# Kernel optimization log

Measured on AMD Instinct MI355X. Metric: run time of the kernel, lower is better.

## Reference

```python
import jax, jax.numpy as jnp
import numpy as np

N = 50000      # nodes
E = 800000     # edges (avg degree 16)
F_IN = 512     # input features
H = 64         # hidden
C = 40         # classes
L = 4          # FAConv layers
EPS = 0.2      # args.epsilon


def setup_inputs() -> dict:
    key = jax.random.key(0)
    ks = jax.random.split(key, 8)
    gain = 1.414
    x = jax.random.normal(ks[0], (N, F_IN), jnp.float32)
    edge_index = jax.random.randint(ks[1], (2, E), 0, N, dtype=jnp.int32)
    W1 = jax.random.normal(ks[2], (H, F_IN), jnp.float32) * (gain * np.sqrt(2.0 / (F_IN + H)))
    b1 = jnp.zeros((H,), jnp.float32)
    W2 = jax.random.normal(ks[3], (C, H), jnp.float32) * (gain * np.sqrt(2.0 / (H + C)))
    b2 = jnp.zeros((C,), jnp.float32)
    att_l = jax.random.normal(ks[4], (L, H), jnp.float32) * np.sqrt(2.0 / (1 + H))
    att_r = jax.random.normal(ks[5], (L, H), jnp.float32) * np.sqrt(2.0 / (1 + H))
    return {"x": x, "edge_index": edge_index, "W1": W1, "b1": b1,
            "W2": W2, "b2": b2, "att_l": att_l, "att_r": att_r}


def reference(x, edge_index, W1, b1, W2, b2, att_l, att_r):
    n = x.shape[0]
    src, dst = edge_index[0], edge_index[1]
    # gcn_norm with self-loops (FAConv normalize=True, add_self_loops=True)
    loop = jnp.arange(n, dtype=src.dtype)
    rows = jnp.concatenate([src, loop])  # source j
    cols = jnp.concatenate([dst, loop])  # target i
    deg = jax.ops.segment_sum(jnp.ones_like(cols, dtype=x.dtype), cols, num_segments=n)
    dinv = jnp.where(deg > 0, jax.lax.rsqrt(jnp.maximum(deg, 1e-12)), 0.0)
    norm = dinv[rows] * dinv[cols]  # [E+N]

    # lin1 + relu (dropout inactive in eval)
    h = jax.nn.relu(x @ W1.T + b1)
    raw = h
    for l in range(L):
        al = h @ att_l[l]  # [N] per-source score
        ar = h @ att_r[l]  # [N] per-target score
        a = jnp.tanh(al[rows] + ar[cols])          # [E+N]
        msg = h[rows] * (a * norm)[:, None]        # [E+N, H]
        h = jax.ops.segment_sum(msg, cols, num_segments=n) + EPS * raw
    logits = h @ W2.T + b2
    return jax.nn.log_softmax(logits, axis=1)
```

## Files before the change

kernel.cpp:

```cpp
#include <hip/hip_runtime.h>

#define F_IN 512
#define HDIM 64
#define NCLS 40
#define NLAYER 4
#define EPS_F 0.2f

typedef __attribute__((ext_vector_type(8))) short short8;
typedef __attribute__((ext_vector_type(4))) float f32x4;
typedef __attribute__((ext_vector_type(8))) unsigned short ushort8;
typedef unsigned long long u64;

__device__ __forceinline__ unsigned short f2bf(float f) {
  unsigned u = __float_as_uint(f);
  u += 0x7FFFu + ((u >> 16) & 1u);
  return (unsigned short)(u >> 16);
}
__device__ __forceinline__ float bf2f(unsigned short s) {
  return __uint_as_float(((unsigned)s) << 16);
}

__global__ __launch_bounds__(256) void k_init(int* indeg, int nN) {
  int i = blockIdx.x * 256 + threadIdx.x;
  if (i < nN) indeg[i] = 0;
}

__global__ __launch_bounds__(256) void k_hist(const int* __restrict__ dst, int* indeg,
                                              int* __restrict__ rank, int nE) {
  int e = blockIdx.x * 256 + threadIdx.x;
  if (e < nE) rank[e] = atomicAdd(&indeg[dst[e]], 1);
}

__global__ __launch_bounds__(256) void k_bsum(const int* __restrict__ indeg, int* bsum, int nN) {
  int i0 = blockIdx.x * 512 + threadIdx.x;
  int v = 0;
  if (i0 < nN) v += indeg[i0];
  if (i0 + 256 < nN) v += indeg[i0 + 256];
#pragma unroll
  for (int off = 32; off > 0; off >>= 1) v += __shfl_xor(v, off, 64);
  __shared__ int s[4];
  if ((threadIdx.x & 63) == 0) s[threadIdx.x >> 6] = v;
  __syncthreads();
  if (threadIdx.x == 0) bsum[blockIdx.x] = s[0] + s[1] + s[2] + s[3];
}

__global__ __launch_bounds__(128) void k_bscan(const int* __restrict__ bsum, int* bpre,
                                               int* rowptr, int nblk, int nN, int nE) {
  __shared__ int sb[128];
  int t = threadIdx.x;
  int v = (t < nblk) ? bsum[t] : 0;
  sb[t] = v;
  __syncthreads();
  int acc = v;
  for (int off = 1; off < 128; off <<= 1) {
    int o = (t >= off) ? sb[t - off] : 0;
    __syncthreads();
    acc += o;
    sb[t] = acc;
    __syncthreads();
  }
  if (t < nblk) bpre[t] = acc - v;
  if (t == 0) rowptr[nN] = nE;
}

__global__ __launch_bounds__(512) void k_rowptr(const int* __restrict__ indeg,
                                                const int* __restrict__ bpre,
                                                const float* __restrict__ al,
                                                const float* __restrict__ ar,
                                                int* rowptr, float* dinv,
                                                float2* P, float2* Q, float* selfc, int nN) {
  __shared__ int sb[512];
  int t = threadIdx.x;
  int i = blockIdx.x * 512 + t;
  int v = (i < nN) ? indeg[i] : 0;
  sb[t] = v;
  __syncthreads();
  int acc = v;
  for (int off = 1; off < 512; off <<= 1) {
    int o = (t >= off) ? sb[t - off] : 0;
    __syncthreads();
    acc += o;
    sb[t] = acc;
    __syncthreads();
  }
  if (i < nN) {
    rowptr[i] = bpre[blockIdx.x] + acc - v;
    float dv = rsqrtf((float)v + 1.0f);
    dinv[i] = dv;
    float a = al[i], r = ar[i];
    P[i] = make_float2(a, dv);
    Q[i] = make_float2(r, dv);
    selfc[i] = tanhf(a + r) * dv * dv;
  }
}

__global__ __launch_bounds__(256) void k_scatter(const int* __restrict__ src,
                                                 const int* __restrict__ dst,
                                                 const int* __restrict__ rank,
                                                 const int* __restrict__ rowptr,
                                                 u64* __restrict__ csr_sd, int nE) {
  int e = blockIdx.x * 256 + threadIdx.x;
  if (e < nE) {
    int s = src[e], d = dst[e];
    int q = rowptr[d] + rank[e];
    csr_sd[q] = ((u64)(unsigned)d << 32) | (u64)(unsigned)s;
  }
}

__global__ __launch_bounds__(256) void k_lin1(const float* __restrict__ x,
                                              const float* __restrict__ W1,
                                              const float* __restrict__ b1,
                                              const float* __restrict__ attl0,
                                              const float* __restrict__ attr0,
                                              unsigned short* __restrict__ hraw,
                                              float* __restrict__ al, float* __restrict__ ar,
                                              int nN) {
  __shared__ unsigned short xs[64 * 64];
  __shared__ unsigned short ws[64 * 64];
  const int t = threadIdx.x;
  const int wv = t >> 6;
  const int l = t & 63;
  const int n0 = blockIdx.x * 64;
  const int srow = t >> 2;
  const int sk4 = (t & 3) * 4;
  const bool xvalid = (n0 + srow) < nN;
  const f32x4* x4 = reinterpret_cast<const f32x4*>(x);
  const f32x4* w4 = reinterpret_cast<const f32x4*>(W1);
  short8* xs8 = reinterpret_cast<short8*>(xs);
  short8* ws8 = reinterpret_cast<short8*>(ws);
  const int wslot0 = srow * 8 + (((t & 3) * 2 + 0) ^ (srow & 7));
  const int wslot1 = srow * 8 + (((t & 3) * 2 + 1) ^ (srow & 7));
  const int arow = l & 15;
  const int kgrp = l >> 4;
  f32x4 acc[4] = {{0.f, 0.f, 0.f, 0.f},
                  {0.f, 0.f, 0.f, 0.f},
                  {0.f, 0.f, 0.f, 0.f},
                  {0.f, 0.f, 0.f, 0.f}};
  f32x4 xa[4], wa[4];
  const f32x4 zero4 = {0.f, 0.f, 0.f, 0.f};
  {
    const size_t xb = (size_t)(n0 + srow) * (F_IN / 4) + sk4;
    const size_t wb = (size_t)srow * (F_IN / 4) + sk4;
#pragma unroll
    for (int r = 0; r < 4; ++r) {
      xa[r] = xvalid ? x4[xb + r] : zero4;
      wa[r] = w4[wb + r];
    }
  }
  for (int c = 0; c < 8; ++c) {
    short8 p0, p1, q0, q1;
#pragma unroll
    for (int r = 0; r < 2; ++r) {
#pragma unroll
      for (int j = 0; j < 4; ++j) {
        p0[r * 4 + j] = (short)f2bf(xa[r][j]);
        p1[r * 4 + j] = (short)f2bf(xa[2 + r][j]);
        q0[r * 4 + j] = (short)f2bf(wa[r][j]);
        q1[r * 4 + j] = (short)f2bf(wa[2 + r][j]);
      }
    }
    xs8[wslot0] = p0;
    xs8[wslot1] = p1;
    ws8[wslot0] = q0;
    ws8[wslot1] = q1;
    __syncthreads();
    if (c < 7) {
      const size_t xb = (size_t)(n0 + srow) * (F_IN / 4) + (c + 1) * 16 + sk4;
      const size_t wb = (size_t)srow * (F_IN / 4) + (c + 1) * 16 + sk4;
#pragma unroll
      for (int r = 0; r < 4; ++r) {
        xa[r] = xvalid ? x4[xb + r] : zero4;
        wa[r] = w4[wb + r];
      }
    }
#pragma unroll
    for (int c2 = 0; c2 < 2; ++c2) {
      const short8 a = xs8[(wv * 16 + arow) * 8 + ((c2 * 4 + kgrp) ^ (arow & 7))];
#pragma unroll
      for (int fs = 0; fs < 4; ++fs) {
        const short8 b = ws8[(fs * 16 + arow) * 8 + ((c2 * 4 + kgrp) ^ (arow & 7))];
        acc[fs] = __builtin_amdgcn_mfma_f32_16x16x32_bf16(a, b, acc[fs], 0, 0, 0);
      }
    }
    __syncthreads();
  }
  float psl[4] = {0.f, 0.f, 0.f, 0.f};
  float psr[4] = {0.f, 0.f, 0.f, 0.f};
#pragma unroll
  for (int fs = 0; fs < 4; ++fs) {
    const int feat = fs * 16 + arow;
    const float bias = b1[feat];
    const float atl = attl0[feat];
    const float atr = attr0[feat];
#pragma unroll
    for (int j = 0; j < 4; ++j) {
      const float v = fmaxf(acc[fs][j] + bias, 0.f);
      const int node = n0 + wv * 16 + kgrp * 4 + j;
      if (node < nN) hraw[(size_t)node * HDIM + feat] = f2bf(v);
      psl[j] = fmaf(v, atl, psl[j]);
      psr[j] = fmaf(v, atr, psr[j]);
    }
  }
#pragma unroll
  for (int off = 1; off <= 8; off <<= 1) {
#pragma unroll
    for (int j = 0; j < 4; ++j) {
      psl[j] += __shfl_xor(psl[j], off, 64);
      psr[j] += __shfl_xor(psr[j], off, 64);
    }
  }
  if (arow == 0) {
#pragma unroll
    for (int j = 0; j < 4; ++j) {
      const int node = n0 + wv * 16 + kgrp * 4 + j;
      if (node < nN) {
        al[node] = psl[j];
        ar[node] = psr[j];
      }
    }
  }
}

__global__ __launch_bounds__(256) void k_coef(const u64* __restrict__ csr_sd,
                                              const float2* __restrict__ P,
                                              const float2* __restrict__ Q,
                                              u64* __restrict__ esc, int nE) {
  int e = blockIdx.x * 256 + threadIdx.x;
  if (e < nE) {
    u64 sd = csr_sd[e];
    int s = (int)(unsigned)(sd & 0xFFFFFFFFull);
    int d = (int)(unsigned)(sd >> 32);
    float2 p = P[s], q = Q[d];
    float c = tanhf(p.x + q.x) * (p.y * q.y);
    esc[e] = ((u64)(unsigned)__float_as_int(c) << 32) | (u64)(unsigned)s;
  }
}

template <bool WNEXT>
__global__ __launch_bounds__(256) void k_agg(const unsigned short* __restrict__ h,
                                             const unsigned short* __restrict__ hraw,
                                             const int* __restrict__ rowptr,
                                             const u64* __restrict__ esc,
                                             const float* __restrict__ dinv,
                                             float* __restrict__ selfc,
                                             const float* __restrict__ attl_n,
                                             const float* __restrict__ attr_n,
                                             float2* __restrict__ P, float2* __restrict__ Q,
                                             unsigned short* __restrict__ hout, int nN) {
  const int wid = threadIdx.x >> 6, lane = threadIdx.x & 63;
  const int d = blockIdx.x * 4 + wid;
  if (d >= nN) return;
  const int grp = lane >> 3;
  const int fo = (lane & 7) * 8;
  const size_t base = (size_t)d * HDIM + fo;
  float acc[8] = {};
  if (grp == 0) {
    const float sc = selfc[d];
    const ushort8 hd = *reinterpret_cast<const ushort8*>(&h[base]);
    const ushort8 rw = *reinterpret_cast<const ushort8*>(&hraw[base]);
#pragma unroll
    for (int j = 0; j < 8; ++j) acc[j] = fmaf(bf2f(hd[j]), sc, EPS_F * bf2f(rw[j]));
  }
  const int e1 = rowptr[d + 1];
  int e = rowptr[d] + grp;
  for (; e + 8 < e1; e += 16) {
    const u64 v0 = esc[e];
    const u64 v1 = esc[e + 8];
    const int s0 = (int)(unsigned)(v0 & 0xFFFFFFFFull);
    const int s1 = (int)(unsigned)(v1 & 0xFFFFFFFFull);
    const ushort8 h0v = *reinterpret_cast<const ushort8*>(&h[(size_t)s0 * HDIM + fo]);
    const ushort8 h1v = *reinterpret_cast<const ushort8*>(&h[(size_t)s1 * HDIM + fo]);
    const float c0 = __int_as_float((int)(v0 >> 32));
    const float c1 = __int_as_float((int)(v1 >> 32));
#pragma unroll
    for (int j = 0; j < 8; ++j) acc[j] = fmaf(bf2f(h0v[j]), c0, acc[j]);
#pragma unroll
    for (int j = 0; j < 8; ++j) acc[j] = fmaf(bf2f(h1v[j]), c1, acc[j]);
  }
  for (; e < e1; e += 8) {
    const u64 v = esc[e];
    const int s = (int)(unsigned)(v & 0xFFFFFFFFull);
    const ushort8 hv = *reinterpret_cast<const ushort8*>(&h[(size_t)s * HDIM + fo]);
    const float c = __int_as_float((int)(v >> 32));
#pragma unroll
    for (int j = 0; j < 8; ++j) acc[j] = fmaf(bf2f(hv[j]), c, acc[j]);
  }
#pragma unroll
  for (int off = 8; off <= 32; off <<= 1) {
#pragma unroll
    for (int j = 0; j < 8; ++j) acc[j] += __shfl_xor(acc[j], off, 64);
  }
  if (grp == 0) {
    ushort8 o;
#pragma unroll
    for (int j = 0; j < 8; ++j) o[j] = f2bf(acc[j]);
    *reinterpret_cast<ushort8*>(&hout[base]) = o;
  }
  if (WNEXT) {
    float psl = 0.f, psr = 0.f;
#pragma unroll
    for (int j = 0; j < 8; ++j) {
      psl = fmaf(acc[j], attl_n[fo + j], psl);
      psr = fmaf(acc[j], attr_n[fo + j], psr);
    }
#pragma unroll
    for (int off = 1; off <= 4; off <<= 1) {
      psl += __shfl_xor(psl, off, 64);
      psr += __shfl_xor(psr, off, 64);
    }
    if (lane == 0) {
      const float dv = dinv[d];
      P[d] = make_float2(psl, dv);
      Q[d] = make_float2(psr, dv);
      selfc[d] = tanhf(psl + psr) * dv * dv;
    }
  }
}

__global__ __launch_bounds__(256) void k_out(const unsigned short* __restrict__ h,
                                             const float* __restrict__ W2,
                                             const float* __restrict__ b2,
                                             float* __restrict__ out, int nN) {
  __shared__ float w2s[NCLS * HDIM];
  __shared__ float b2s[NCLS];
  for (int i = threadIdx.x; i < NCLS * HDIM; i += 256) w2s[i] = W2[i];
  if (threadIdx.x < NCLS) b2s[threadIdx.x] = b2[threadIdx.x];
  __syncthreads();
  const int n = blockIdx.x * 256 + threadIdx.x;
  if (n >= nN) return;
  float hr[HDIM];
  const ushort8* hrow = reinterpret_cast<const ushort8*>(&h[(size_t)n * HDIM]);
#pragma unroll
  for (int r = 0; r < 8; ++r) {
    const ushort8 v = hrow[r];
#pragma unroll
    for (int j = 0; j < 8; ++j) hr[r * 8 + j] = bf2f(v[j]);
  }
  const float4* w2s4 = reinterpret_cast<const float4*>(w2s);
  float logits[NCLS];
  float m = -INFINITY;
#pragma unroll
  for (int c = 0; c < NCLS; ++c) {
    float a0 = 0.f, a1 = 0.f, a2 = 0.f, a3 = 0.f;
#pragma unroll
    for (int j4 = 0; j4 < HDIM / 4; j4 += 4) {
      const float4 w0 = w2s4[c * (HDIM / 4) + j4 + 0];
      const float4 w1 = w2s4[c * (HDIM / 4) + j4 + 1];
      const float4 w2v = w2s4[c * (HDIM / 4) + j4 + 2];
      const float4 w3 = w2s4[c * (HDIM / 4) + j4 + 3];
      const int j = j4 * 4;
      a0 = fmaf(hr[j + 0], w0.x, a0);  a0 = fmaf(hr[j + 1], w0.y, a0);
      a0 = fmaf(hr[j + 2], w0.z, a0);  a0 = fmaf(hr[j + 3], w0.w, a0);
      a1 = fmaf(hr[j + 4], w1.x, a1);  a1 = fmaf(hr[j + 5], w1.y, a1);
      a1 = fmaf(hr[j + 6], w1.z, a1);  a1 = fmaf(hr[j + 7], w1.w, a1);
      a2 = fmaf(hr[j + 8], w2v.x, a2); a2 = fmaf(hr[j + 9], w2v.y, a2);
      a2 = fmaf(hr[j + 10], w2v.z, a2); a2 = fmaf(hr[j + 11], w2v.w, a2);
      a3 = fmaf(hr[j + 12], w3.x, a3); a3 = fmaf(hr[j + 13], w3.y, a3);
      a3 = fmaf(hr[j + 14], w3.z, a3); a3 = fmaf(hr[j + 15], w3.w, a3);
    }
    const float lg = (a0 + a1) + (a2 + a3) + b2s[c];
    logits[c] = lg;
    m = fmaxf(m, lg);
  }
  float s = 0.f;
#pragma unroll
  for (int c = 0; c < NCLS; ++c) s += expf(logits[c] - m);
  const float lse = m + logf(s);
  float4* o4 = reinterpret_cast<float4*>(&out[(size_t)n * NCLS]);
#pragma unroll
  for (int c4 = 0; c4 < NCLS / 4; ++c4) {
    float4 o;
    o.x = logits[c4 * 4 + 0] - lse;
    o.y = logits[c4 * 4 + 1] - lse;
    o.z = logits[c4 * 4 + 2] - lse;
    o.w = logits[c4 * 4 + 3] - lse;
    o4[c4] = o;
  }
}

extern "C" void kernel_launch(void* const* d_in, const int* in_sizes, int n_in,
                              void* d_out, int out_size, void* d_ws, size_t ws_size,
                              hipStream_t stream) {
  const float* x = (const float*)d_in[0];
  const int* ei = (const int*)d_in[1];
  const float* W1 = (const float*)d_in[2];
  const float* b1 = (const float*)d_in[3];
  const float* W2 = (const float*)d_in[4];
  const float* b2 = (const float*)d_in[5];
  const float* attl = (const float*)d_in[6];
  const float* attr = (const float*)d_in[7];
  float* out = (float*)d_out;

  const int nN = in_sizes[0] / F_IN;
  const int nE = in_sizes[1] / 2;
  const int* src = ei;
  const int* dst = ei + nE;

  char* w = (char*)d_ws;
  size_t off = 0;
  auto alloc = [&](size_t bytes) {
    void* p = (void*)(w + off);
    off = (off + bytes + 255) & ~(size_t)255;
    return p;
  };
  unsigned short* hraw = (unsigned short*)alloc((size_t)nN * HDIM * 2);
  unsigned short* hA = (unsigned short*)alloc((size_t)nN * HDIM * 2);
  unsigned short* hB = (unsigned short*)alloc((size_t)nN * HDIM * 2);
  float2* P = (float2*)alloc((size_t)nN * 8);
  float2* Q = (float2*)alloc((size_t)nN * 8);
  float* selfc = (float*)alloc((size_t)nN * 4);
  float* dinv = (float*)alloc((size_t)nN * 4);
  float* al = (float*)alloc((size_t)nN * 4);
  float* ar = (float*)alloc((size_t)nN * 4);
  int* indeg = (int*)alloc((size_t)nN * 4);
  int* rank = (int*)alloc((size_t)nE * 4);
  int* rowptr = (int*)alloc((size_t)(nN + 1) * 4);
  u64* csr_sd = (u64*)alloc((size_t)nE * 8);
  u64* esc = (u64*)alloc((size_t)nE * 8);
  int* bsum = (int*)alloc(1024);
  int* bpre = (int*)alloc(1024);

  const int nb_n = (nN + 255) / 256;
  const int nb_e = (nE + 255) / 256;
  const int nblk = (nN + 511) / 512;
  const int nb4 = (nN + 3) / 4;

  k_lin1<<<(nN + 63) / 64, 256, 0, stream>>>(x, W1, b1, attl, attr, hraw, al, ar, nN);
  k_init<<<nb_n, 256, 0, stream>>>(indeg, nN);
  k_hist<<<nb_e, 256, 0, stream>>>(dst, indeg, rank, nE);
  k_bsum<<<nblk, 256, 0, stream>>>(indeg, bsum, nN);
  k_bscan<<<1, 128, 0, stream>>>(bsum, bpre, rowptr, nblk, nN, nE);
  k_rowptr<<<nblk, 512, 0, stream>>>(indeg, bpre, al, ar, rowptr, dinv, P, Q, selfc, nN);
  k_scatter<<<nb_e, 256, 0, stream>>>(src, dst, rank, rowptr, csr_sd, nE);

  const unsigned short* hin = hraw;
  unsigned short* hout = hA;
  for (int l = 0; l < NLAYER; ++l) {
    k_coef<<<nb_e, 256, 0, stream>>>(csr_sd, P, Q, esc, nE);
    if (l < NLAYER - 1) {
      k_agg<true><<<nb4, 256, 0, stream>>>(hin, hraw, rowptr, esc, dinv, selfc,
                                           attl + (l + 1) * HDIM, attr + (l + 1) * HDIM,
                                           P, Q, hout, nN);
    } else {
      k_agg<false><<<nb4, 256, 0, stream>>>(hin, hraw, rowptr, esc, dinv, selfc,
                                            nullptr, nullptr, P, Q, hout, nN);
    }
    hin = hout;
    hout = (hout == hA) ? hB : hA;
  }
  k_out<<<nb_n, 256, 0, stream>>>(hin, W2, b2, out, nN);
}
```

Measured before the change: 260.3 us.

## Split hidden features into two half-planes, fuse edge coefficients into aggregation

Stores hidden features as two planar halves of 32 features each. Every layer now runs two aggregation passes, one per half, so the gather working set per pass is half the size and more likely to stay in cache. The separate edge-coefficient kernel and its 64-bit esc array are removed: the tanh coefficient is recomputed inline from P and Q inside each pass. CSR now holds only source indices, and the next-layer attention scores are built from per-pass partial sums kept in scratch. The costs are duplicated rowptr/csrsrc/P traffic and tanh work across the two passes, double-buffered P/Q/S arrays, and one more launch per layer.

```diff
diff --git a/kernel.cpp b/kernel.cpp
--- a/kernel.cpp
+++ b/kernel.cpp
@@ -67,7 +67,7 @@
                                                 const int* __restrict__ bpre,
                                                 const float* __restrict__ al,
                                                 const float* __restrict__ ar,
-                                                int* rowptr, float* dinv,
+                                                int* rowptr,
                                                 float2* P, float2* Q, float* selfc, int nN) {
   __shared__ int sb[512];
   int t = threadIdx.x;
@@ -86,7 +86,6 @@
   if (i < nN) {
     rowptr[i] = bpre[blockIdx.x] + acc - v;
     float dv = rsqrtf((float)v + 1.0f);
-    dinv[i] = dv;
     float a = al[i], r = ar[i];
     P[i] = make_float2(a, dv);
     Q[i] = make_float2(r, dv);
@@ -98,12 +97,11 @@
                                                  const int* __restrict__ dst,
                                                  const int* __restrict__ rank,
                                                  const int* __restrict__ rowptr,
-                                                 u64* __restrict__ csr_sd, int nE) {
+                                                 int* __restrict__ csrsrc, int nE) {
   int e = blockIdx.x * 256 + threadIdx.x;
   if (e < nE) {
-    int s = src[e], d = dst[e];
-    int q = rowptr[d] + rank[e];
-    csr_sd[q] = ((u64)(unsigned)d << 32) | (u64)(unsigned)s;
+    int d = dst[e];
+    csrsrc[rowptr[d] + rank[e]] = src[e];
   }
 }
 
@@ -132,6 +130,7 @@
   const int wslot1 = srow * 8 + (((t & 3) * 2 + 1) ^ (srow & 7));
   const int arow = l & 15;
   const int kgrp = l >> 4;
+  const size_t PL = (size_t)nN * 32;
   f32x4 acc[4] = {{0.f, 0.f, 0.f, 0.f},
                   {0.f, 0.f, 0.f, 0.f},
                   {0.f, 0.f, 0.f, 0.f},
@@ -192,11 +191,12 @@
     const float bias = b1[feat];
     const float atl = attl0[feat];
     const float atr = attr0[feat];
+    const size_t pbase = (size_t)(fs >> 1) * PL + (size_t)((fs & 1) * 16 + arow);
 #pragma unroll
     for (int j = 0; j < 4; ++j) {
       const float v = fmaxf(acc[fs][j] + bias, 0.f);
       const int node = n0 + wv * 16 + kgrp * 4 + j;
-      if (node < nN) hraw[(size_t)node * HDIM + feat] = f2bf(v);
+      if (node < nN) hraw[pbase + (size_t)node * 32] = f2bf(v);
       psl[j] = fmaf(v, atl, psl[j]);
       psr[j] = fmaf(v, atr, psr[j]);
     }
@@ -221,72 +221,46 @@
   }
 }
 
-__global__ __launch_bounds__(256) void k_coef(const u64* __restrict__ csr_sd,
-                                              const float2* __restrict__ P,
-                                              const float2* __restrict__ Q,
-                                              u64* __restrict__ esc, int nE) {
-  int e = blockIdx.x * 256 + threadIdx.x;
-  if (e < nE) {
-    u64 sd = csr_sd[e];
-    int s = (int)(unsigned)(sd & 0xFFFFFFFFull);
-    int d = (int)(unsigned)(sd >> 32);
-    float2 p = P[s], q = Q[d];
-    float c = tanhf(p.x + q.x) * (p.y * q.y);
-    esc[e] = ((u64)(unsigned)__float_as_int(c) << 32) | (u64)(unsigned)s;
-  }
-}
-
-template <bool WNEXT>
-__global__ __launch_bounds__(256) void k_agg(const unsigned short* __restrict__ h,
-                                             const unsigned short* __restrict__ hraw,
+template <int PASS, bool WNEXT>
+__global__ __launch_bounds__(256) void k_agg(const unsigned short* __restrict__ hin_p,
+                                             const unsigned short* __restrict__ hraw_p,
                                              const int* __restrict__ rowptr,
-                                             const u64* __restrict__ esc,
-                                             const float* __restrict__ dinv,
-                                             float* __restrict__ selfc,
-                                             const float* __restrict__ attl_n,
-                                             const float* __restrict__ attr_n,
-                                             float2* __restrict__ P, float2* __restrict__ Q,
-                                             unsigned short* __restrict__ hout, int nN) {
+                                             const int* __restrict__ csrsrc,
+                                             const float2* __restrict__ Pc,
+                                             const float2* __restrict__ Qc,
+                                             const float* __restrict__ Sc,
+                                             const float* __restrict__ attl_h,
+                                             const float* __restrict__ attr_h,
+                                             float* __restrict__ psl_s, float* __restrict__ psr_s,
+                                             float2* __restrict__ Pn, float2* __restrict__ Qn,
+                                             float* __restrict__ Sn,
+                                             unsigned short* __restrict__ hout_p, int nN) {
   const int wid = threadIdx.x >> 6, lane = threadIdx.x & 63;
   const int d = blockIdx.x * 4 + wid;
   if (d >= nN) return;
-  const int grp = lane >> 3;
-  const int fo = (lane & 7) * 8;
-  const size_t base = (size_t)d * HDIM + fo;
+  const int grp = lane >> 2;
+  const int fo = (lane & 3) * 8;
+  const size_t base = (size_t)d * 32 + fo;
+  const float2 qd = Qc[d];
   float acc[8] = {};
   if (grp == 0) {
-    const float sc = selfc[d];
-    const ushort8 hd = *reinterpret_cast<const ushort8*>(&h[base]);
-    const ushort8 rw = *reinterpret_cast<const ushort8*>(&hraw[base]);
+    const float sc = Sc[d];
+    const ushort8 hd = *reinterpret_cast<const ushort8*>(&hin_p[base]);
+    const ushort8 rw = *reinterpret_cast<const ushort8*>(&hraw_p[base]);
 #pragma unroll
     for (int j = 0; j < 8; ++j) acc[j] = fmaf(bf2f(hd[j]), sc, EPS_F * bf2f(rw[j]));
   }
-  const int e1 = rowptr[d + 1];
-  int e = rowptr[d] + grp;
-  for (; e + 8 < e1; e += 16) {
-    const u64 v0 = esc[e];
-    const u64 v1 = esc[e + 8];
-    const int s0 = (int)(unsigned)(v0 & 0xFFFFFFFFull);
-    const int s1 = (int)(unsigned)(v1 & 0xFFFFFFFFull);
-    const ushort8 h0v = *reinterpret_cast<const ushort8*>(&h[(size_t)s0 * HDIM + fo]);
-    const ushort8 h1v = *reinterpret_cast<const ushort8*>(&h[(size_t)s1 * HDIM + fo]);
-    const float c0 = __int_as_float((int)(v0 >> 32));
-    const float c1 = __int_as_float((int)(v1 >> 32));
-#pragma unroll
-    for (int j = 0; j < 8; ++j) acc[j] = fmaf(bf2f(h0v[j]), c0, acc[j]);
-#pragma unroll
-    for (int j = 0; j < 8; ++j) acc[j] = fmaf(bf2f(h1v[j]), c1, acc[j]);
-  }
-  for (; e < e1; e += 8) {
-    const u64 v = esc[e];
-    const int s = (int)(unsigned)(v & 0xFFFFFFFFull);
-    const ushort8 hv = *reinterpret_cast<const ushort8*>(&h[(size_t)s * HDIM + fo]);
-    const float c = __int_as_float((int)(v >> 32));
+  const int r1 = rowptr[d + 1];
+  for (int e = rowptr[d] + grp; e < r1; e += 16) {
+    const int s = csrsrc[e];
+    const float2 p = Pc[s];
+    const ushort8 hv = *reinterpret_cast<const ushort8*>(&hin_p[(size_t)s * 32 + fo]);
+    const float c = tanhf(p.x + qd.x) * (p.y * qd.y);
 #pragma unroll
     for (int j = 0; j < 8; ++j) acc[j] = fmaf(bf2f(hv[j]), c, acc[j]);
   }
 #pragma unroll
-  for (int off = 8; off <= 32; off <<= 1) {
+  for (int off = 4; off <= 32; off <<= 1) {
 #pragma unroll
     for (int j = 0; j < 8; ++j) acc[j] += __shfl_xor(acc[j], off, 64);
   }
@@ -294,25 +268,30 @@
     ushort8 o;
 #pragma unroll
     for (int j = 0; j < 8; ++j) o[j] = f2bf(acc[j]);
-    *reinterpret_cast<ushort8*>(&hout[base]) = o;
+    *reinterpret_cast<ushort8*>(&hout_p[base]) = o;
   }
   if (WNEXT) {
     float psl = 0.f, psr = 0.f;
 #pragma unroll
     for (int j = 0; j < 8; ++j) {
-      psl = fmaf(acc[j], attl_n[fo + j], psl);
-      psr = fmaf(acc[j], attr_n[fo + j], psr);
-    }
-#pragma unroll
-    for (int off = 1; off <= 4; off <<= 1) {
-      psl += __shfl_xor(psl, off, 64);
-      psr += __shfl_xor(psr, off, 64);
-    }
+      psl = fmaf(acc[j], attl_h[fo + j], psl);
+      psr = fmaf(acc[j], attr_h[fo + j], psr);
+    }
+    psl += __shfl_xor(psl, 1, 64);
+    psl += __shfl_xor(psl, 2, 64);
+    psr += __shfl_xor(psr, 1, 64);
+    psr += __shfl_xor(psr, 2, 64);
     if (lane == 0) {
-      const float dv = dinv[d];
-      P[d] = make_float2(psl, dv);
-      Q[d] = make_float2(psr, dv);
-      selfc[d] = tanhf(psl + psr) * dv * dv;
+      if (PASS == 0) {
+        psl_s[d] = psl;
+        psr_s[d] = psr;
+      } else {
+        psl += psl_s[d];
+        psr += psr_s[d];
+        Pn[d] = make_float2(psl, qd.y);
+        Qn[d] = make_float2(psr, qd.y);
+        Sn[d] = tanhf(psl + psr) * qd.y * qd.y;
+      }
     }
   }
 }
@@ -328,13 +307,21 @@
   __syncthreads();
   const int n = blockIdx.x * 256 + threadIdx.x;
   if (n >= nN) return;
+  const size_t PL = (size_t)nN * 32;
   float hr[HDIM];
-  const ushort8* hrow = reinterpret_cast<const ushort8*>(&h[(size_t)n * HDIM]);
-#pragma unroll
-  for (int r = 0; r < 8; ++r) {
-    const ushort8 v = hrow[r];
+  const ushort8* lo = reinterpret_cast<const ushort8*>(&h[(size_t)n * 32]);
+  const ushort8* hi = reinterpret_cast<const ushort8*>(&h[PL + (size_t)n * 32]);
+#pragma unroll
+  for (int r = 0; r < 4; ++r) {
+    const ushort8 v = lo[r];
 #pragma unroll
     for (int j = 0; j < 8; ++j) hr[r * 8 + j] = bf2f(v[j]);
+  }
+#pragma unroll
+  for (int r = 0; r < 4; ++r) {
+    const ushort8 v = hi[r];
+#pragma unroll
+    for (int j = 0; j < 8; ++j) hr[32 + r * 8 + j] = bf2f(v[j]);
   }
   const float4* w2s4 = reinterpret_cast<const float4*>(w2s);
   float logits[NCLS];
@@ -395,6 +382,7 @@
   const int nE = in_sizes[1] / 2;
   const int* src = ei;
   const int* dst = ei + nE;
+  const size_t PL = (size_t)nN * 32;
 
   char* w = (char*)d_ws;
   size_t off = 0;
@@ -406,17 +394,18 @@
   unsigned short* hraw = (unsigned short*)alloc((size_t)nN * HDIM * 2);
   unsigned short* hA = (unsigned short*)alloc((size_t)nN * HDIM * 2);
   unsigned short* hB = (unsigned short*)alloc((size_t)nN * HDIM * 2);
-  float2* P = (float2*)alloc((size_t)nN * 8);
-  float2* Q = (float2*)alloc((size_t)nN * 8);
-  float* selfc = (float*)alloc((size_t)nN * 4);
-  float* dinv = (float*)alloc((size_t)nN * 4);
+  float2* P0 = (float2*)alloc((size_t)nN * 8);
+  float2* Q0 = (float2*)alloc((size_t)nN * 8);
+  float* S0 = (float*)alloc((size_t)nN * 4);
+  float2* P1 = (float2*)alloc((size_t)nN * 8);
+  float2* Q1 = (float2*)alloc((size_t)nN * 8);
+  float* S1 = (float*)alloc((size_t)nN * 4);
   float* al = (float*)alloc((size_t)nN * 4);
   float* ar = (float*)alloc((size_t)nN * 4);
   int* indeg = (int*)alloc((size_t)nN * 4);
   int* rank = (int*)alloc((size_t)nE * 4);
   int* rowptr = (int*)alloc((size_t)(nN + 1) * 4);
-  u64* csr_sd = (u64*)alloc((size_t)nE * 8);
-  u64* esc = (u64*)alloc((size_t)nE * 8);
+  int* csrsrc = (int*)alloc((size_t)nE * 4);
   int* bsum = (int*)alloc(1024);
   int* bpre = (int*)alloc(1024);
 
@@ -430,23 +419,34 @@
   k_hist<<<nb_e, 256, 0, stream>>>(dst, indeg, rank, nE);
   k_bsum<<<nblk, 256, 0, stream>>>(indeg, bsum, nN);
   k_bscan<<<1, 128, 0, stream>>>(bsum, bpre, rowptr, nblk, nN, nE);
-  k_rowptr<<<nblk, 512, 0, stream>>>(indeg, bpre, al, ar, rowptr, dinv, P, Q, selfc, nN);
-  k_scatter<<<nb_e, 256, 0, stream>>>(src, dst, rank, rowptr, csr_sd, nE);
+  k_rowptr<<<nblk, 512, 0, stream>>>(indeg, bpre, al, ar, rowptr, P0, Q0, S0, nN);
+  k_scatter<<<nb_e, 256, 0, stream>>>(src, dst, rank, rowptr, csrsrc, nE);
 
   const unsigned short* hin = hraw;
   unsigned short* hout = hA;
+  float2 *Pc = P0, *Qc = Q0, *Pn = P1, *Qn = Q1;
+  float *Sc = S0, *Sn = S1;
   for (int l = 0; l < NLAYER; ++l) {
-    k_coef<<<nb_e, 256, 0, stream>>>(csr_sd, P, Q, esc, nE);
+    const float* atl_n = attl + (l + 1) * HDIM;
+    const float* atr_n = attr + (l + 1) * HDIM;
     if (l < NLAYER - 1) {
-      k_agg<true><<<nb4, 256, 0, stream>>>(hin, hraw, rowptr, esc, dinv, selfc,
-                                           attl + (l + 1) * HDIM, attr + (l + 1) * HDIM,
-                                           P, Q, hout, nN);
+      k_agg<0, true><<<nb4, 256, 0, stream>>>(hin, hraw, rowptr, csrsrc, Pc, Qc, Sc,
+                                              atl_n, atr_n, al, ar, Pn, Qn, Sn, hout, nN);
+      k_agg<1, true><<<nb4, 256, 0, stream>>>(hin + PL, hraw + PL, rowptr, csrsrc, Pc, Qc, Sc,
+                                              atl_n + 32, atr_n + 32, al, ar, Pn, Qn, Sn,
+                                              hout + PL, nN);
     } else {
-      k_agg<false><<<nb4, 256, 0, stream>>>(hin, hraw, rowptr, esc, dinv, selfc,
-                                            nullptr, nullptr, P, Q, hout, nN);
+      k_agg<0, false><<<nb4, 256, 0, stream>>>(hin, hraw, rowptr, csrsrc, Pc, Qc, Sc,
+                                               nullptr, nullptr, al, ar, Pn, Qn, Sn, hout, nN);
+      k_agg<1, false><<<nb4, 256, 0, stream>>>(hin + PL, hraw + PL, rowptr, csrsrc, Pc, Qc, Sc,
+                                               nullptr, nullptr, al, ar, Pn, Qn, Sn,
+                                               hout + PL, nN);
     }
     hin = hout;
     hout = (hout == hA) ? hB : hA;
+    float2* tp = Pc; Pc = Pn; Pn = tp;
+    float2* tq = Qc; Qc = Qn; Qn = tq;
+    float* ts = Sc; Sc = Sn; Sn = ts;
   }
   k_out<<<nb_n, 256, 0, stream>>>(hin, W2, b2, out, nN);
 }
```

Result: slower. 330.0 us (+26.8%).

## Fuse edge coefficient computation into aggregation and shrink CSR to source indices

Applied to the files above, without the earlier changes.

Removes the per-layer k_coef kernel, which wrote a packed coefficient and source array for every edge. The aggregation kernel now reads 4-byte source indices and computes tanh(al+ar)*dinv_s*dinv_d inline from per-node P/Q arrays, which are double-buffered so that next-layer writes do not race with current reads. This saves four launches and the write and read of an 8-byte-per-edge array each layer, in exchange for an extra random 8-byte gather of P per edge and redundant tanh evaluation across the 8 lanes of each group. The separate dinv array is dropped and taken from Q.y.

```diff
diff --git a/kernel.cpp b/kernel.cpp
--- a/kernel.cpp
+++ b/kernel.cpp
@@ -67,7 +67,7 @@
                                                 const int* __restrict__ bpre,
                                                 const float* __restrict__ al,
                                                 const float* __restrict__ ar,
-                                                int* rowptr, float* dinv,
+                                                int* rowptr,
                                                 float2* P, float2* Q, float* selfc, int nN) {
   __shared__ int sb[512];
   int t = threadIdx.x;
@@ -86,7 +86,6 @@
   if (i < nN) {
     rowptr[i] = bpre[blockIdx.x] + acc - v;
     float dv = rsqrtf((float)v + 1.0f);
-    dinv[i] = dv;
     float a = al[i], r = ar[i];
     P[i] = make_float2(a, dv);
     Q[i] = make_float2(r, dv);
@@ -98,12 +97,11 @@
                                                  const int* __restrict__ dst,
                                                  const int* __restrict__ rank,
                                                  const int* __restrict__ rowptr,
-                                                 u64* __restrict__ csr_sd, int nE) {
+                                                 int* __restrict__ csrsrc, int nE) {
   int e = blockIdx.x * 256 + threadIdx.x;
   if (e < nE) {
-    int s = src[e], d = dst[e];
-    int q = rowptr[d] + rank[e];
-    csr_sd[q] = ((u64)(unsigned)d << 32) | (u64)(unsigned)s;
+    int d = dst[e];
+    csrsrc[rowptr[d] + rank[e]] = src[e];
   }
 }
 
@@ -221,31 +219,18 @@
   }
 }
 
-__global__ __launch_bounds__(256) void k_coef(const u64* __restrict__ csr_sd,
-                                              const float2* __restrict__ P,
-                                              const float2* __restrict__ Q,
-                                              u64* __restrict__ esc, int nE) {
-  int e = blockIdx.x * 256 + threadIdx.x;
-  if (e < nE) {
-    u64 sd = csr_sd[e];
-    int s = (int)(unsigned)(sd & 0xFFFFFFFFull);
-    int d = (int)(unsigned)(sd >> 32);
-    float2 p = P[s], q = Q[d];
-    float c = tanhf(p.x + q.x) * (p.y * q.y);
-    esc[e] = ((u64)(unsigned)__float_as_int(c) << 32) | (u64)(unsigned)s;
-  }
-}
-
 template <bool WNEXT>
 __global__ __launch_bounds__(256) void k_agg(const unsigned short* __restrict__ h,
                                              const unsigned short* __restrict__ hraw,
                                              const int* __restrict__ rowptr,
-                                             const u64* __restrict__ esc,
-                                             const float* __restrict__ dinv,
-                                             float* __restrict__ selfc,
+                                             const int* __restrict__ csrsrc,
+                                             const float2* __restrict__ Pc,
+                                             const float2* __restrict__ Qc,
+                                             const float* __restrict__ Sc,
                                              const float* __restrict__ attl_n,
                                              const float* __restrict__ attr_n,
-                                             float2* __restrict__ P, float2* __restrict__ Q,
+                                             float2* __restrict__ Pn, float2* __restrict__ Qn,
+                                             float* __restrict__ Sn,
                                              unsigned short* __restrict__ hout, int nN) {
   const int wid = threadIdx.x >> 6, lane = threadIdx.x & 63;
   const int d = blockIdx.x * 4 + wid;
@@ -253,9 +238,10 @@
   const int grp = lane >> 3;
   const int fo = (lane & 7) * 8;
   const size_t base = (size_t)d * HDIM + fo;
+  const float2 qd = Qc[d];
   float acc[8] = {};
   if (grp == 0) {
-    const float sc = selfc[d];
+    const float sc = Sc[d];
     const ushort8 hd = *reinterpret_cast<const ushort8*>(&h[base]);
     const ushort8 rw = *reinterpret_cast<const ushort8*>(&hraw[base]);
 #pragma unroll
@@ -264,24 +250,24 @@
   const int e1 = rowptr[d + 1];
   int e = rowptr[d] + grp;
   for (; e + 8 < e1; e += 16) {
-    const u64 v0 = esc[e];
-    const u64 v1 = esc[e + 8];
-    const int s0 = (int)(unsigned)(v0 & 0xFFFFFFFFull);
-    const int s1 = (int)(unsigned)(v1 & 0xFFFFFFFFull);
+    const int s0 = csrsrc[e];
+    const int s1 = csrsrc[e + 8];
+    const float2 p0 = Pc[s0];
+    const float2 p1 = Pc[s1];
     const ushort8 h0v = *reinterpret_cast<const ushort8*>(&h[(size_t)s0 * HDIM + fo]);
     const ushort8 h1v = *reinterpret_cast<const ushort8*>(&h[(size_t)s1 * HDIM + fo]);
-    const float c0 = __int_as_float((int)(v0 >> 32));
-    const float c1 = __int_as_float((int)(v1 >> 32));
+    const float c0 = tanhf(p0.x + qd.x) * (p0.y * qd.y);
+    const float c1 = tanhf(p1.x + qd.x) * (p1.y * qd.y);
 #pragma unroll
     for (int j = 0; j < 8; ++j) acc[j] = fmaf(bf2f(h0v[j]), c0, acc[j]);
 #pragma unroll
     for (int j = 0; j < 8; ++j) acc[j] = fmaf(bf2f(h1v[j]), c1, acc[j]);
   }
   for (; e < e1; e += 8) {
-    const u64 v = esc[e];
-    const int s = (int)(unsigned)(v & 0xFFFFFFFFull);
+    const int s = csrsrc[e];
+    const float2 p = Pc[s];
     const ushort8 hv = *reinterpret_cast<const ushort8*>(&h[(size_t)s * HDIM + fo]);
-    const float c = __int_as_float((int)(v >> 32));
+    const float c = tanhf(p.x + qd.x) * (p.y * qd.y);
 #pragma unroll
     for (int j = 0; j < 8; ++j) acc[j] = fmaf(bf2f(hv[j]), c, acc[j]);
   }
@@ -309,10 +295,9 @@
       psr += __shfl_xor(psr, off, 64);
     }
     if (lane == 0) {
-      const float dv = dinv[d];
-      P[d] = make_float2(psl, dv);
-      Q[d] = make_float2(psr, dv);
-      selfc[d] = tanhf(psl + psr) * dv * dv;
+      Pn[d] = make_float2(psl, qd.y);
+      Qn[d] = make_float2(psr, qd.y);
+      Sn[d] = tanhf(psl + psr) * qd.y * qd.y;
     }
   }
 }
@@ -406,17 +391,18 @@
   unsigned short* hraw = (unsigned short*)alloc((size_t)nN * HDIM * 2);
   unsigned short* hA = (unsigned short*)alloc((size_t)nN * HDIM * 2);
   unsigned short* hB = (unsigned short*)alloc((size_t)nN * HDIM * 2);
-  float2* P = (float2*)alloc((size_t)nN * 8);
-  float2* Q = (float2*)alloc((size_t)nN * 8);
-  float* selfc = (float*)alloc((size_t)nN * 4);
-  float* dinv = (float*)alloc((size_t)nN * 4);
+  float2* P0 = (float2*)alloc((size_t)nN * 8);
+  float2* Q0 = (float2*)alloc((size_t)nN * 8);
+  float* S0 = (float*)alloc((size_t)nN * 4);
+  float2* P1 = (float2*)alloc((size_t)nN * 8);
+  float2* Q1 = (float2*)alloc((size_t)nN * 8);
+  float* S1 = (float*)alloc((size_t)nN * 4);
   float* al = (float*)alloc((size_t)nN * 4);
   float* ar = (float*)alloc((size_t)nN * 4);
   int* indeg = (int*)alloc((size_t)nN * 4);
   int* rank = (int*)alloc((size_t)nE * 4);
   int* rowptr = (int*)alloc((size_t)(nN + 1) * 4);
-  u64* csr_sd = (u64*)alloc((size_t)nE * 8);
-  u64* esc = (u64*)alloc((size_t)nE * 8);
+  int* csrsrc = (int*)alloc((size_t)nE * 4);
   int* bsum = (int*)alloc(1024);
   int* bpre = (int*)alloc(1024);
 
@@ -430,23 +416,27 @@
   k_hist<<<nb_e, 256, 0, stream>>>(dst, indeg, rank, nE);
   k_bsum<<<nblk, 256, 0, stream>>>(indeg, bsum, nN);
   k_bscan<<<1, 128, 0, stream>>>(bsum, bpre, rowptr, nblk, nN, nE);
-  k_rowptr<<<nblk, 512, 0, stream>>>(indeg, bpre, al, ar, rowptr, dinv, P, Q, selfc, nN);
-  k_scatter<<<nb_e, 256, 0, stream>>>(src, dst, rank, rowptr, csr_sd, nE);
+  k_rowptr<<<nblk, 512, 0, stream>>>(indeg, bpre, al, ar, rowptr, P0, Q0, S0, nN);
+  k_scatter<<<nb_e, 256, 0, stream>>>(src, dst, rank, rowptr, csrsrc, nE);
 
   const unsigned short* hin = hraw;
   unsigned short* hout = hA;
+  float2 *Pc = P0, *Qc = Q0, *Pn = P1, *Qn = Q1;
+  float *Sc = S0, *Sn = S1;
   for (int l = 0; l < NLAYER; ++l) {
-    k_coef<<<nb_e, 256, 0, stream>>>(csr_sd, P, Q, esc, nE);
     if (l < NLAYER - 1) {
-      k_agg<true><<<nb4, 256, 0, stream>>>(hin, hraw, rowptr, esc, dinv, selfc,
+      k_agg<true><<<nb4, 256, 0, stream>>>(hin, hraw, rowptr, csrsrc, Pc, Qc, Sc,
                                            attl + (l + 1) * HDIM, attr + (l + 1) * HDIM,
-                                           P, Q, hout, nN);
+                                           Pn, Qn, Sn, hout, nN);
     } else {
-      k_agg<false><<<nb4, 256, 0, stream>>>(hin, hraw, rowptr, esc, dinv, selfc,
-                                            nullptr, nullptr, P, Q, hout, nN);
+      k_agg<false><<<nb4, 256, 0, stream>>>(hin, hraw, rowptr, csrsrc, Pc, Qc, Sc,
+                                            nullptr, nullptr, Pn, Qn, Sn, hout, nN);
     }
     hin = hout;
     hout = (hout == hA) ? hB : hA;
+    float2* tp = Pc; Pc = Pn; Pn = tp;
+    float2* tq = Qc; Qc = Qn; Qn = tq;
+    float* ts = Sc; Sc = Sn; Sn = ts;
   }
   k_out<<<nb_n, 256, 0, stream>>>(hin, W2, b2, out, nN);
 }
```

After: 238.2 us. 8.5% less time.
